# Optimization experiments

Measured on AMD Instinct MI355X. Metric: run time of the kernel, lower is better.

The kernel has to match this reference:

```python
import jax, jax.numpy as jnp
import numpy as np

B, N, M, K = 8, 9225, 4096, 32
D = 2          # coordinate dim
HID = 64       # MLP hidden
DOUT = 16      # MLP output / f_y channels


def setup_inputs() -> dict:
    key = jax.random.key(0)
    ks = jax.random.split(key, 10)
    y = jax.random.uniform(ks[0], (B, N, D), dtype=jnp.float32)
    x = jax.random.uniform(ks[1], (B, M, D), dtype=jnp.float32)
    f_y = jax.random.uniform(ks[2], (B, N, DOUT), dtype=jnp.float32)
    weights = jax.random.uniform(ks[3], (B, N), dtype=jnp.float32)
    neighbors_index = jax.random.randint(ks[4], (B, M, K), 0, N, dtype=jnp.int64)
    drop = jax.random.uniform(ks[5], (B, M, K)) < 0.1
    neighbors_index = jnp.where(drop, jnp.int64(-1), neighbors_index)
    # LinearChannelMLP params: 4 -> 64 -> 16, gelu between
    W1 = jax.random.normal(ks[6], (2 * D, HID), dtype=jnp.float32) * (1.0 / np.sqrt(2 * D))
    b1 = jnp.zeros((HID,), dtype=jnp.float32)
    W2 = jax.random.normal(ks[7], (HID, DOUT), dtype=jnp.float32) * (1.0 / np.sqrt(HID))
    b2 = jnp.zeros((DOUT,), dtype=jnp.float32)
    return {"y": y, "x": x, "f_y": f_y, "weights": weights,
            "W1": W1, "b1": b1, "W2": W2, "b2": b2,
            "neighbors_index": neighbors_index}


def _batched_gather(table, idx):
    # table: [B, N, ...], idx: [B, M, K] -> [B, M, K, ...]
    return jax.vmap(lambda t, i: t[i])(table, idx)


def reference(y, x, f_y, weights, W1, b1, W2, b2, neighbors_index):
    idx = jnp.where(neighbors_index == -1, 0, neighbors_index)      # [B,M,K]
    valid = (neighbors_index != -1).astype(y.dtype)[..., None]      # [B,M,K,1]

    rep_y = _batched_gather(y, idx)                                 # [B,M,K,D]
    in_f = _batched_gather(f_y, idx)                                # [B,M,K,DOUT]
    self_x = jnp.broadcast_to(x[:, :, None, :], rep_y.shape)        # [B,M,K,D]

    agg = jnp.concatenate([rep_y, self_x], axis=-1)                 # [B,M,K,2D]
    h = jax.nn.gelu(agg @ W1 + b1, approximate=False)               # [B,M,K,HID]
    kval = h @ W2 + b2                                              # [B,M,K,DOUT]

    kval = kval * in_f                                              # linear transform: k(x,y)*f(y)
    w_nbr = _batched_gather(weights, idx)[..., None]                # [B,M,K,1]
    kval = kval * w_nbr * valid
    return kval.sum(axis=2)                                         # [B,M,DOUT]
```

## Files before the change

### kernel.cpp

```cpp
#include <hip/hip_runtime.h>
#include <hip/hip_bf16.h>

#define B_    8
#define N_    9225
#define M_    4096
#define K_    32
#define HID_  64
#define DOUT_ 16

typedef __attribute__((ext_vector_type(8))) short short8;
typedef __attribute__((ext_vector_type(4))) float floatx4;
typedef __attribute__((ext_vector_type(2))) float f32x2;

static __device__ __forceinline__ short f2bf(float f) {
    __hip_bfloat16 h = __float2bfloat16(f);
    return __builtin_bit_cast(short, h);
}
static __device__ __forceinline__ f32x2 splat2(float v) { return (f32x2){v, v}; }
static __device__ __forceinline__ int bpermi(int src_bytes, int v) {
    return __builtin_amdgcn_ds_bpermute(src_bytes, v);
}
static __device__ __forceinline__ float bpermf(int src_bytes, float v) {
    return __builtin_bit_cast(float,
        __builtin_amdgcn_ds_bpermute(src_bytes, __builtin_bit_cast(int, v)));
}

static __device__ __forceinline__ float row16_sum(float v) {
    int t;
    t = __builtin_amdgcn_update_dpp(0, __builtin_bit_cast(int, v), 0x111, 0xF, 0xF, true);
    v += __builtin_bit_cast(float, t);
    t = __builtin_amdgcn_update_dpp(0, __builtin_bit_cast(int, v), 0x112, 0xF, 0xF, true);
    v += __builtin_bit_cast(float, t);
    t = __builtin_amdgcn_update_dpp(0, __builtin_bit_cast(int, v), 0x114, 0xF, 0xF, true);
    v += __builtin_bit_cast(float, t);
    t = __builtin_amdgcn_update_dpp(0, __builtin_bit_cast(int, v), 0x118, 0xF, 0xF, true);
    v += __builtin_bit_cast(float, t);
    return v;
}

static __device__ __forceinline__ f32x2 gelu2(f32x2 x) {
    const f32x2 xsq = x * x;
    const f32x2 t   = __builtin_elementwise_fma(xsq, splat2(0.035677408f), splat2(0.79788456f));
    const f32x2 z   = x * t;
    const f32x2 u   = z * z;
    const f32x2 a   = u + splat2(105.0f);
    const f32x2 nin = __builtin_elementwise_fma(u, a, splat2(945.0f));
    const f32x2 num = z * nin;
    const f32x2 bq  = __builtin_elementwise_fma(u, splat2(15.0f), splat2(420.0f));
    const f32x2 den = __builtin_elementwise_fma(u, bq, splat2(945.0f));
    const f32x2 r   = { __builtin_amdgcn_rcpf(den[0]), __builtin_amdgcn_rcpf(den[1]) };
    f32x2 th = num * r;
    th = __builtin_elementwise_min(__builtin_elementwise_max(th, splat2(-1.0f)), splat2(1.0f));
    const f32x2 hx = x * splat2(0.5f);
    return __builtin_elementwise_fma(hx, th, hx);
}

__global__ __launch_bounds__(256) void it_kernel(
    const float* __restrict__ y,
    const float* __restrict__ x,
    const float* __restrict__ f_y,
    const float* __restrict__ weights,
    const float* __restrict__ W1,
    const float* __restrict__ b1,
    const float* __restrict__ W2,
    const float* __restrict__ b2,
    const int*   __restrict__ nbr,
    float*       __restrict__ out)
{
    const int tid  = threadIdx.x;
    const int lane = tid & 63;
    const int q    = lane >> 4;
    const int nlo  = lane & 15;
    const int blk   = blockIdx.x;
    const int batch = blk & 7;
    const int pidx  = (blk >> 3) * 4 + (tid >> 6);
    const int row0  = __builtin_amdgcn_readfirstlane(batch * M_ + pidx * 2);
    const int bbase = batch * N_;

    const int r_g = lane >> 5, kk = lane & 31;
    const int raw = nbr[(size_t)(row0 + r_g) * K_ + kk];
    const int vld = raw >= 0;
    const int bn_g = bbase + (vld ? raw : 0);
    const float2 yvg = *(const float2*)(y + (size_t)bn_g * 2);
    const float  wg  = vld ? weights[bn_g] : 0.0f;

    short8 a1f[4];
    #pragma unroll
    for (int t = 0; t < 4; ++t) {
        #pragma unroll
        for (int jj = 0; jj < 8; ++jj) {
            const int k = q * 8 + jj;
            float v = 0.0f;
            if (k < 4)       v = W1[k * 64 + t * 16 + nlo];
            else if (k == 4) v = b1[t * 16 + nlo];
            a1f[t][jj] = f2bf(v);
        }
    }

    short8 w2f[2];
    #pragma unroll
    for (int ch = 0; ch < 2; ++ch)
        #pragma unroll
        for (int jj = 0; jj < 8; ++jj) {
            const int j = (ch * 2 + (jj >> 2)) * 16 + q * 4 + (jj & 3);
            w2f[ch][jj] = f2bf(W2[j * DOUT_ + nlo]);
        }

    const floatx4 b2v = *(const floatx4*)(b2 + q * 4);
    const short one_bf = f2bf(1.0f);

    float partial[4] = {0.f, 0.f, 0.f, 0.f};
    #pragma unroll
    for (int ph = 0; ph < 4; ++ph) {
        const int it = ph >> 1, h = ph & 1;
        const int src = ((it << 5) + (h << 4) + nlo) << 2;

        const int bn = bpermi(src, bn_g);
        const floatx4 fv = *(const floatx4*)(f_y + (size_t)bn * 16 + q * 4);

        f32x2 yv;
        yv[0] = bpermf(src, yvg.x);
        yv[1] = bpermf(src, yvg.y);
        const float s = bpermf(src, wg);
        const float2 xv = *(const float2*)(x + (size_t)(row0 + it) * 2);

        short8 bfrag = {0, 0, 0, 0, 0, 0, 0, 0};
        if (q == 0) {
            bfrag[0] = f2bf(yv[0]);
            bfrag[1] = f2bf(yv[1]);
            bfrag[2] = f2bf(xv.x);
            bfrag[3] = f2bf(xv.y);
            bfrag[4] = one_bf;
        }

        floatx4 accT[4];
        #pragma unroll
        for (int t = 0; t < 4; ++t) {
            floatx4 z4 = {0.f, 0.f, 0.f, 0.f};
            accT[t] = __builtin_amdgcn_mfma_f32_16x16x32_bf16(a1f[t], bfrag, z4, 0, 0, 0);
        }

        short8 hf[2];
        #pragma unroll
        for (int ch = 0; ch < 2; ++ch)
            #pragma unroll
            for (int half = 0; half < 2; ++half) {
                const floatx4 a = accT[ch * 2 + half];
                const f32x2 g0 = gelu2((f32x2){a[0], a[1]});
                const f32x2 g1 = gelu2((f32x2){a[2], a[3]});
                hf[ch][half * 4 + 0] = f2bf(g0[0]);
                hf[ch][half * 4 + 1] = f2bf(g0[1]);
                hf[ch][half * 4 + 2] = f2bf(g1[0]);
                hf[ch][half * 4 + 3] = f2bf(g1[1]);
            }

        floatx4 acc = b2v;
        acc = __builtin_amdgcn_mfma_f32_16x16x32_bf16(w2f[0], hf[0], acc, 0, 0, 0);
        acc = __builtin_amdgcn_mfma_f32_16x16x32_bf16(w2f[1], hf[1], acc, 0, 0, 0);
        #pragma unroll
        for (int r4 = 0; r4 < 4; ++r4)
            partial[r4] = fmaf(acc[r4], fv[r4] * s, partial[r4]);

        if (h == 1) {
            #pragma unroll
            for (int r4 = 0; r4 < 4; ++r4)
                partial[r4] = row16_sum(partial[r4]);
            if (nlo == 15) {
                floatx4 o = {partial[0], partial[1], partial[2], partial[3]};
                *(floatx4*)(out + (size_t)(row0 + it) * DOUT_ + q * 4) = o;
            }
            #pragma unroll
            for (int r4 = 0; r4 < 4; ++r4) partial[r4] = 0.f;
        }
    }
}

extern "C" void kernel_launch(void* const* d_in, const int* in_sizes, int n_in,
                              void* d_out, int out_size, void* d_ws, size_t ws_size,
                              hipStream_t stream) {
    const float* y   = (const float*)d_in[0];
    const float* x   = (const float*)d_in[1];
    const float* f_y = (const float*)d_in[2];
    const float* w   = (const float*)d_in[3];
    const float* W1  = (const float*)d_in[4];
    const float* b1  = (const float*)d_in[5];
    const float* W2  = (const float*)d_in[6];
    const float* b2  = (const float*)d_in[7];
    const int*   nbr = (const int*)d_in[8];
    float* out = (float*)d_out;

    dim3 grid(B_ * M_ / 8), block(256);
    hipLaunchKernelGGL(it_kernel, grid, block, 0, stream,
                       y, x, f_y, w, W1, b1, W2, b2, nbr, out);
}
```

Measured before the change: 106.5 us.

## Pack per-point f_y, y and weight into one gathered record via prep kernel

A new prep kernel writes, for every source point, a 64-byte record split into four 16-byte quarters. Each quarter holds bf16-packed f_y channels, bf16 y coordinates and the fp32 weight, and an extra zeroed sentinel record stands in for padded neighbors. The main kernel then gathers a single uint4 per lane instead of separate f_y, y and weight loads plus ds_bpermute broadcasts, and the x loads are hoisted out of the loop. The cost is an extra kernel launch and a full pass over f_y/y/weights every call, plus f_y is rounded to bf16, which lowers accuracy of the final product.

```diff
diff --git a/kernel.cpp b/kernel.cpp
--- a/kernel.cpp
+++ b/kernel.cpp
@@ -7,6 +7,7 @@
 #define K_    32
 #define HID_  64
 #define DOUT_ 16
+#define SENT  (B_ * N_)
 
 typedef __attribute__((ext_vector_type(8))) short short8;
 typedef __attribute__((ext_vector_type(4))) float floatx4;
@@ -16,13 +17,14 @@
     __hip_bfloat16 h = __float2bfloat16(f);
     return __builtin_bit_cast(short, h);
 }
+static __device__ __forceinline__ unsigned pack2bf(float a, float b) {
+    const unsigned lo = (unsigned)(unsigned short)__builtin_bit_cast(short, __float2bfloat16(a));
+    const unsigned hi = (unsigned)(unsigned short)__builtin_bit_cast(short, __float2bfloat16(b));
+    return (hi << 16) | lo;
+}
 static __device__ __forceinline__ f32x2 splat2(float v) { return (f32x2){v, v}; }
 static __device__ __forceinline__ int bpermi(int src_bytes, int v) {
     return __builtin_amdgcn_ds_bpermute(src_bytes, v);
-}
-static __device__ __forceinline__ float bpermf(int src_bytes, float v) {
-    return __builtin_bit_cast(float,
-        __builtin_amdgcn_ds_bpermute(src_bytes, __builtin_bit_cast(int, v)));
 }
 
 static __device__ __forceinline__ float row16_sum(float v) {
@@ -55,17 +57,36 @@
     return __builtin_elementwise_fma(hx, th, hx);
 }
 
+__global__ __launch_bounds__(256) void prep_kernel(
+    const float* __restrict__ y,
+    const float* __restrict__ f_y,
+    const float* __restrict__ w,
+    unsigned*    __restrict__ pack)
+{
+    const int t = blockIdx.x * 256 + threadIdx.x;
+    const int n = t >> 2, c = t & 3;
+    if (n > SENT) return;
+    uint4 o = {0u, 0u, 0u, 0u};
+    if (n < SENT) {
+        const floatx4 f = *(const floatx4*)(f_y + (size_t)n * 16 + c * 4);
+        o.x = pack2bf(f[0], f[1]);
+        o.y = pack2bf(f[2], f[3]);
+        const float2 yv = *(const float2*)(y + (size_t)n * 2);
+        o.z = pack2bf(yv.x, yv.y);
+        o.w = __builtin_bit_cast(unsigned, w[n]);
+    }
+    *(uint4*)(pack + (size_t)n * 16 + c * 4) = o;
+}
+
 __global__ __launch_bounds__(256) void it_kernel(
-    const float* __restrict__ y,
-    const float* __restrict__ x,
-    const float* __restrict__ f_y,
-    const float* __restrict__ weights,
-    const float* __restrict__ W1,
-    const float* __restrict__ b1,
-    const float* __restrict__ W2,
-    const float* __restrict__ b2,
-    const int*   __restrict__ nbr,
-    float*       __restrict__ out)
+    const float*    __restrict__ x,
+    const float*    __restrict__ W1,
+    const float*    __restrict__ b1,
+    const float*    __restrict__ W2,
+    const float*    __restrict__ b2,
+    const int*      __restrict__ nbr,
+    const unsigned* __restrict__ pack,
+    float*          __restrict__ out)
 {
     const int tid  = threadIdx.x;
     const int lane = tid & 63;
@@ -79,10 +100,7 @@
 
     const int r_g = lane >> 5, kk = lane & 31;
     const int raw = nbr[(size_t)(row0 + r_g) * K_ + kk];
-    const int vld = raw >= 0;
-    const int bn_g = bbase + (vld ? raw : 0);
-    const float2 yvg = *(const float2*)(y + (size_t)bn_g * 2);
-    const float  wg  = vld ? weights[bn_g] : 0.0f;
+    const int bn_g = (raw >= 0) ? (bbase + raw) : SENT;
 
     short8 a1f[4];
     #pragma unroll
@@ -109,6 +127,11 @@
     const floatx4 b2v = *(const floatx4*)(b2 + q * 4);
     const short one_bf = f2bf(1.0f);
 
+    const float2 xv0 = *(const float2*)(x + (size_t)row0 * 2);
+    const float2 xv1 = *(const float2*)(x + (size_t)row0 * 2 + 2);
+    const short xb[2][2] = { { f2bf(xv0.x), f2bf(xv0.y) },
+                             { f2bf(xv1.x), f2bf(xv1.y) } };
+
     float partial[4] = {0.f, 0.f, 0.f, 0.f};
     #pragma unroll
     for (int ph = 0; ph < 4; ++ph) {
@@ -116,20 +139,20 @@
         const int src = ((it << 5) + (h << 4) + nlo) << 2;
 
         const int bn = bpermi(src, bn_g);
-        const floatx4 fv = *(const floatx4*)(f_y + (size_t)bn * 16 + q * 4);
-
-        f32x2 yv;
-        yv[0] = bpermf(src, yvg.x);
-        yv[1] = bpermf(src, yvg.y);
-        const float s = bpermf(src, wg);
-        const float2 xv = *(const float2*)(x + (size_t)(row0 + it) * 2);
+        const uint4 rec = *(const uint4*)(pack + (size_t)bn * 16 + q * 4);
+
+        const float fv0 = __builtin_bit_cast(float, rec.x << 16);
+        const float fv1 = __builtin_bit_cast(float, rec.x & 0xffff0000u);
+        const float fv2 = __builtin_bit_cast(float, rec.y << 16);
+        const float fv3 = __builtin_bit_cast(float, rec.y & 0xffff0000u);
+        const float s   = __builtin_bit_cast(float, rec.w);
 
         short8 bfrag = {0, 0, 0, 0, 0, 0, 0, 0};
         if (q == 0) {
-            bfrag[0] = f2bf(yv[0]);
-            bfrag[1] = f2bf(yv[1]);
-            bfrag[2] = f2bf(xv.x);
-            bfrag[3] = f2bf(xv.y);
+            bfrag[0] = (short)(rec.z & 0xffffu);
+            bfrag[1] = (short)(rec.z >> 16);
+            bfrag[2] = xb[it][0];
+            bfrag[3] = xb[it][1];
             bfrag[4] = one_bf;
         }
 
@@ -157,9 +180,10 @@
         floatx4 acc = b2v;
         acc = __builtin_amdgcn_mfma_f32_16x16x32_bf16(w2f[0], hf[0], acc, 0, 0, 0);
         acc = __builtin_amdgcn_mfma_f32_16x16x32_bf16(w2f[1], hf[1], acc, 0, 0, 0);
-        #pragma unroll
-        for (int r4 = 0; r4 < 4; ++r4)
-            partial[r4] = fmaf(acc[r4], fv[r4] * s, partial[r4]);
+        partial[0] = fmaf(acc[0], fv0 * s, partial[0]);
+        partial[1] = fmaf(acc[1], fv1 * s, partial[1]);
+        partial[2] = fmaf(acc[2], fv2 * s, partial[2]);
+        partial[3] = fmaf(acc[3], fv3 * s, partial[3]);
 
         if (h == 1) {
             #pragma unroll
@@ -188,8 +212,13 @@
     const float* b2  = (const float*)d_in[7];
     const int*   nbr = (const int*)d_in[8];
     float* out = (float*)d_out;
+    unsigned* pack = (unsigned*)d_ws;
+
+    const int nthread = (SENT + 1) * 4;
+    dim3 pgrid((nthread + 255) / 256), pblock(256);
+    hipLaunchKernelGGL(prep_kernel, pgrid, pblock, 0, stream, y, f_y, w, pack);
 
     dim3 grid(B_ * M_ / 8), block(256);
     hipLaunchKernelGGL(it_kernel, grid, block, 0, stream,
-                       y, x, f_y, w, W1, b1, W2, b2, nbr, out);
-}
+                       x, W1, b1, W2, b2, nbr, pack, out);
+}
```

Result: slower. 110.9 us (+4.2%).
